# Performance work log

Measured on AMD Instinct MI355X. Metric: run time of the kernel, lower is better.

Reference implementation:

```python
import jax, jax.numpy as jnp
import numpy as np
import math

B, T, C = 2, 8192, 1024
H = 16
HD = C // H  # 64
WIN = 256    # local_window_size


def _rope_tables(T, hd):
    inv_freq = 1.0 / (10000.0 ** (np.arange(0, hd, 2, dtype=np.float32) / hd))
    t = np.arange(T, dtype=np.float32)
    freqs = np.outer(t, inv_freq)                      # [T, hd/2]
    emb = np.concatenate([freqs, freqs], axis=-1)      # [T, hd]
    return jnp.asarray(np.cos(emb))[None, None], jnp.asarray(np.sin(emb))[None, None]


def setup_inputs() -> dict:
    key = jax.random.key(0)
    ks = jax.random.split(key, 10)
    x = jax.random.normal(ks[0], (B, T, C), dtype=jnp.float32)
    # padding_mask: bool [B,T]; per the source, True positions end up masked out of attention
    padding_mask = jax.random.randint(ks[1], (B, T), 0, 2).astype(bool)
    cos, sin = _rope_tables(T, HD)                     # [1,1,T,HD]
    s = 1.0 / math.sqrt(C)
    Wq = jax.random.normal(ks[2], (C, C), dtype=jnp.float32) * s
    bq = jnp.zeros((C,), dtype=jnp.float32)
    Wk = jax.random.normal(ks[3], (C, C), dtype=jnp.float32) * s
    bk = jnp.zeros((C,), dtype=jnp.float32)
    Wv = jax.random.normal(ks[4], (C, C), dtype=jnp.float32) * s
    bv = jnp.zeros((C,), dtype=jnp.float32)
    Wo = jax.random.normal(ks[5], (C, C), dtype=jnp.float32) * s
    bo = jnp.zeros((C,), dtype=jnp.float32)
    return {"x": x, "padding_mask": padding_mask, "cos": cos, "sin": sin,
            "Wq": Wq, "bq": bq, "Wk": Wk, "bk": bk, "Wv": Wv, "bv": bv,
            "Wo": Wo, "bo": bo}


def _rotate_half(t):
    h = t.shape[-1] // 2
    return jnp.concatenate([-t[..., h:], t[..., :h]], axis=-1)


def reference(x, padding_mask, cos, sin, Wq, bq, Wk, bk, Wv, bv, Wo, bo):
    Bx, Tx, Cx = x.shape
    Wn = WIN
    pad_end = (Wn - Tx % Wn) % Wn            # static python int
    Tp = Tx + pad_end
    nW = Tp // Wn
    half = Wn // 2
    hd = cos.shape[-1]

    cos_t = jnp.broadcast_to(cos[0, 0][None], (Bx, Tx, hd))
    sin_t = jnp.broadcast_to(sin[0, 0][None], (Bx, Tx, hd))
    if pad_end > 0:
        x = jnp.pad(x, ((0, 0), (0, pad_end), (0, 0)))
        padding_mask = jnp.pad(padding_mask, ((0, 0), (0, pad_end)))
        cos_t = jnp.pad(cos_t, ((0, 0), (0, pad_end), (0, 0)))
        sin_t = jnp.pad(sin_t, ((0, 0), (0, pad_end), (0, 0)))

    # non-overlapping query windows: [B*nW, W, C]
    q_win = x.reshape(Bx * nW, Wn, Cx)
    cos_q = cos_t.reshape(Bx * nW, Wn, hd)[:, None]   # [Bw,1,W,hd]
    sin_q = sin_t.reshape(Bx * nW, Wn, hd)[:, None]

    # overlapping key/value windows of size 2W, stride W
    x_ctx = jnp.pad(x, ((0, 0), (half, half), (0, 0)))
    cos_ctx = jnp.pad(cos_t, ((0, 0), (half, half), (0, 0)))
    sin_ctx = jnp.pad(sin_t, ((0, 0), (half, half), (0, 0)))
    pk = jnp.pad(padding_mask, ((0, 0), (half, half)))  # pad value False
    idx = jnp.arange(nW)[:, None] * Wn + jnp.arange(2 * Wn)[None, :]  # [nW, 2W]
    k_win = x_ctx[:, idx].reshape(Bx * nW, 2 * Wn, Cx)
    cos_k = cos_ctx[:, idx].reshape(Bx * nW, 2 * Wn, hd)[:, None]
    sin_k = sin_ctx[:, idx].reshape(Bx * nW, 2 * Wn, hd)[:, None]
    pk = pk[:, idx].reshape(Bx * nW, 2 * Wn)

    # attn_mask: True = attend (SDPA bool-mask convention)
    attn_mask = ~pk
    all_attend = jnp.all(attn_mask, axis=-1)
    attn_mask = attn_mask.at[:, 0].set(jnp.where(all_attend, False, attn_mask[:, 0]))

    Bw = Bx * nW
    q = (q_win @ Wq.T + bq).reshape(Bw, Wn, H, HD).transpose(0, 2, 1, 3)        # [Bw,H,W,hd]
    k = (k_win @ Wk.T + bk).reshape(Bw, 2 * Wn, H, HD).transpose(0, 2, 1, 3)    # [Bw,H,2W,hd]
    v = (k_win @ Wv.T + bv).reshape(Bw, 2 * Wn, H, HD).transpose(0, 2, 1, 3)

    q = q * cos_q + _rotate_half(q) * sin_q
    k = k * cos_k + _rotate_half(k) * sin_k

    scale = 1.0 / math.sqrt(HD)
    scores = jnp.einsum('bhqd,bhkd->bhqk', q, k) * scale                        # [Bw,H,W,2W]
    scores = jnp.where(attn_mask[:, None, None, :], scores, jnp.finfo(scores.dtype).min)
    attn = jax.nn.softmax(scores, axis=-1)
    out = jnp.einsum('bhqk,bhkd->bhqd', attn, v)
    out = out.transpose(0, 2, 1, 3).reshape(Bw, Wn, Cx)
    out = out @ Wo.T + bo
    out = out.reshape(Bx, nW * Wn, Cx)[:, :Tx]
    return out
```

## Files before the change

### kernel.cpp

```cpp
#include <hip/hip_runtime.h>
#include <hip/hip_bf16.h>
#include <stdint.h>

#define T_SEQ 8192
#define B_SZ 2
#define CDIM 1024
#define NH 16
#define HDIM 64
#define NW 32

typedef unsigned short ushort_t;
typedef __attribute__((ext_vector_type(8))) short short8;
typedef __attribute__((ext_vector_type(8))) unsigned short us8;
typedef __attribute__((ext_vector_type(4))) unsigned short us4;
typedef __attribute__((ext_vector_type(4))) float f32x4;

__device__ __forceinline__ unsigned short f2bf(float f) {
  union { float f; unsigned int u; } c; c.f = f;
  return (unsigned short)((c.u + 0x7FFFu + ((c.u >> 16) & 1u)) >> 16);
}
__device__ __forceinline__ unsigned pk2(float a, float b) {
  unsigned r;
  asm("v_cvt_pk_bf16_f32 %0, %1, %2" : "=v"(r) : "v"(a), "v"(b));
  return r;
}
__device__ __forceinline__ void gld16(void* lds, const void* g) {
  __builtin_amdgcn_global_load_lds(
      (const __attribute__((address_space(1))) void*)g,
      (__attribute__((address_space(3))) void*)lds, 16, 0, 0);
}

__global__ __launch_bounds__(256) void cvt_all(const float* __restrict__ x,
                                               const float* __restrict__ w0,
                                               const float* __restrict__ w1,
                                               const float* __restrict__ w2,
                                               const float* __restrict__ w3,
                                               ushort_t* __restrict__ xbf,
                                               ushort_t* __restrict__ wbf,
                                               int nx4)
{
  int i = blockIdx.x * 256 + threadIdx.x;
  const float* src;
  ushort_t* dst;
  int idx;
  if (i < nx4) {
    src = x; dst = xbf; idx = i;
  } else {
    int j = i - nx4;
    int mat = j >> 18;
    idx = j & 262143;
    src = (mat == 0) ? w0 : (mat == 1) ? w1 : (mat == 2) ? w2 : w3;
    dst = wbf + (size_t)mat * CDIM * CDIM;
  }
  float4 v = ((const float4*)src)[idx];
  ushort4 o;
  o.x = f2bf(v.x); o.y = f2bf(v.y); o.z = f2bf(v.z); o.w = f2bf(v.w);
  ((ushort4*)dst)[idx] = o;
}

__device__ __forceinline__ void gemm256_core(const ushort_t* __restrict__ A,
                                             const ushort_t* __restrict__ W,
                                             ushort_t* SH,
                                             int m0, int n0, int t, f32x4 acc[8][4])
{
  const int lane = t & 63;
  const int wv = t >> 6;
  const int wr = wv >> 2;
  const int wc = wv & 3;
  const int fr = lane & 15;
  const int quad = lane >> 4;

  ushort_t* As = SH;
  ushort_t* Bs = SH + 32768;

  const int sr8 = lane >> 3;
  const int scb = ((lane & 7) ^ sr8) * 8;
  const int srowb = wv * 8 + sr8;
  const ushort_t* Ag = A + (size_t)(m0 + srowb) * CDIM + scb;
  const ushort_t* Wg = W + (size_t)(n0 + srowb) * CDIM + scb;
  ushort_t* lA = As + srowb * 64 + (lane & 7) * 8;
  ushort_t* lB = Bs + srowb * 64 + (lane & 7) * 8;

#pragma unroll
  for (int p = 0; p < 4; p++) {
    gld16(lA + p * 4096, Ag + (size_t)p * 64 * CDIM);
    gld16(lB + p * 4096, Wg + (size_t)p * 64 * CDIM);
  }
  __syncthreads();

  for (int kt = 0; kt < CDIM / 64; ++kt) {
    const int cur = kt & 1;
    if (kt + 1 < CDIM / 64) {
      const ushort_t* Agn = Ag + (kt + 1) * 64;
      const ushort_t* Wgn = Wg + (kt + 1) * 64;
      ushort_t* nA = lA + (cur ^ 1) * 16384;
      ushort_t* nB = lB + (cur ^ 1) * 16384;
#pragma unroll
      for (int p = 0; p < 4; p++) {
        gld16(nA + p * 4096, Agn + (size_t)p * 64 * CDIM);
        gld16(nB + p * 4096, Wgn + (size_t)p * 64 * CDIM);
      }
    }
    const ushort_t* Ac = As + cur * 16384;
    const ushort_t* Bc = Bs + cur * 16384;
    short8 b[4][2];
#pragma unroll
    for (int j = 0; j < 4; j++)
#pragma unroll
      for (int ks = 0; ks < 2; ks++)
        b[j][ks] = *(const short8*)&Bc[(wc * 64 + j * 16 + fr) * 64 +
                                       (((ks * 4 + quad) ^ (fr & 7)) * 8)];
    __builtin_amdgcn_s_setprio(1);
#pragma unroll
    for (int i = 0; i < 8; i++) {
      const int ra = (wr * 128 + i * 16 + fr) * 64;
      short8 a0 = *(const short8*)&Ac[ra + ((quad ^ (fr & 7)) * 8)];
      short8 a1 = *(const short8*)&Ac[ra + (((4 + quad) ^ (fr & 7)) * 8)];
#pragma unroll
      for (int j = 0; j < 4; j++)
        acc[i][j] = __builtin_amdgcn_mfma_f32_16x16x32_bf16(a0, b[j][0], acc[i][j], 0, 0, 0);
#pragma unroll
      for (int j = 0; j < 4; j++)
        acc[i][j] = __builtin_amdgcn_mfma_f32_16x16x32_bf16(a1, b[j][1], acc[i][j], 0, 0, 0);
    }
    __builtin_amdgcn_s_setprio(0);
    __syncthreads();
  }
}

__device__ __forceinline__ void xcd_swz(int& bx, int& by) {
  int gx = gridDim.x, nwg = gx * gridDim.y;
  int lid = bx + gx * by;
  int cpx = nwg >> 3;
  int swz = (lid & 7) * cpx + (lid >> 3);
  bx = swz % gx;
  by = swz / gx;
}

__global__ __launch_bounds__(512, 1) void gemm_qkv(const ushort_t* __restrict__ A,
                                                   const ushort_t* __restrict__ Wcat,
                                                   const float* __restrict__ bq,
                                                   const float* __restrict__ bk,
                                                   const float* __restrict__ bv,
                                                   ushort_t* __restrict__ Qb,
                                                   ushort_t* __restrict__ Kb,
                                                   ushort_t* __restrict__ Vtb,
                                                   const float* __restrict__ cosT,
                                                   const float* __restrict__ sinT)
{
  extern __shared__ ushort_t SH[];

  const int t = threadIdx.x;
  const int lane = t & 63;
  const int wv = t >> 6;
  const int wr = wv >> 2;
  const int wc = wv & 3;
  const int fr = lane & 15;
  const int quad = lane >> 4;
  int bx = blockIdx.x, by = blockIdx.y;
  xcd_swz(bx, by);
  const int m0 = by * 256;
  const int n0 = bx * 256;
  const int sec = bx >> 2;
  const int nsec0 = (bx & 3) * 256;
  const float* bias = (sec == 0) ? bq : (sec == 1) ? bk : bv;

  f32x4 acc[8][4];
#pragma unroll
  for (int i = 0; i < 8; i++)
#pragma unroll
    for (int j = 0; j < 4; j++) acc[i][j] = (f32x4){0.f, 0.f, 0.f, 0.f};

  gemm256_core(A, Wcat, SH, m0, n0, t, acc);

  if (sec < 2) {
    ushort_t* OutQK = sec ? Kb : Qb;
#pragma unroll
    for (int half = 0; half < 2; ++half) {
      if (wr == half) {
#pragma unroll
        for (int jp = 0; jp < 2; jp++) {
          int d = jp * 16 + fr;
          int cl = wc * 64 + jp * 16 + fr;
          float bl = bias[nsec0 + cl];
          float bh = bias[nsec0 + cl + 32];
#pragma unroll
          for (int i = 0; i < 8; i++) {
            int rloc = i * 16 + quad * 4;
#pragma unroll
            for (int r = 0; r < 4; r++) {
              int m = m0 + half * 128 + rloc + r;
              int tt = m & (T_SEQ - 1);
              float c = cosT[tt * HDIM + d];
              float sn = sinT[tt * HDIM + d];
              float lo = acc[i][jp][r] + bl;
              float hi = acc[i][jp + 2][r] + bh;
              SH[(rloc + r) * 264 + cl] = f2bf(lo * c - hi * sn);
              SH[(rloc + r) * 264 + cl + 32] = f2bf(hi * c + lo * sn);
            }
          }
        }
      }
      __syncthreads();
      const int rr0 = t >> 5;
      const int c8 = (t & 31) * 8;
      size_t gbase = (size_t)(m0 + half * 128) * CDIM + nsec0 + c8;
#pragma unroll
      for (int pp = 0; pp < 8; pp++) {
        int rr = pp * 16 + rr0;
        *(us8*)&OutQK[gbase + (size_t)rr * CDIM] = *(const us8*)&SH[rr * 264 + c8];
      }
      __syncthreads();
    }
  } else {
#pragma unroll
    for (int j = 0; j < 4; j++) {
      int ch = nsec0 + wc * 64 + j * 16 + fr;
      float bvv = bias[ch];
#pragma unroll
      for (int i = 0; i < 8; i++) {
        int m = m0 + wr * 128 + i * 16 + quad * 4;
        int bb = m >> 13;
        int tq = m & (T_SEQ - 1);
        us4 pk;
#pragma unroll
        for (int r = 0; r < 4; r++) pk[r] = f2bf(acc[i][j][r] + bvv);
        *(us4*)&Vtb[((size_t)bb * CDIM + ch) * T_SEQ + tq] = pk;
      }
    }
  }
}

__global__ __launch_bounds__(512, 1) void gemm_out(const ushort_t* __restrict__ A,
                                                   const ushort_t* __restrict__ W,
                                                   const float* __restrict__ bias,
                                                   float* __restrict__ Out)
{
  extern __shared__ ushort_t SH[];

  const int t = threadIdx.x;
  const int lane = t & 63;
  const int wv = t >> 6;
  const int wr = wv >> 2;
  const int wc = wv & 3;
  const int fr = lane & 15;
  const int quad = lane >> 4;
  int bx = blockIdx.x, by = blockIdx.y;
  xcd_swz(bx, by);
  const int m0 = by * 256;
  const int n0 = bx * 256;

  f32x4 acc[8][4];
#pragma unroll
  for (int i = 0; i < 8; i++)
#pragma unroll
    for (int j = 0; j < 4; j++) acc[i][j] = (f32x4){0.f, 0.f, 0.f, 0.f};

  gemm256_core(A, W, SH, m0, n0, t, acc);

#pragma unroll
  for (int j = 0; j < 4; j++) {
    int n = n0 + wc * 64 + j * 16 + fr;
    float bvv = bias[n];
#pragma unroll
    for (int i = 0; i < 8; i++) {
      int m = m0 + wr * 128 + i * 16 + quad * 4;
#pragma unroll
      for (int r = 0; r < 4; r++)
        Out[(size_t)(m + r) * CDIM + n] = acc[i][j][r] + bvv;
    }
  }
}

__global__ __launch_bounds__(256, 4) void attn_kernel(const ushort_t* __restrict__ Q,
                                                      const ushort_t* __restrict__ Kg,
                                                      const ushort_t* __restrict__ Vt,
                                                      const int* __restrict__ mask,
                                                      ushort_t* __restrict__ AO)
{
  __shared__ ushort_t Ks[64 * 72];
  __shared__ ushort_t Vts[64 * 72];
  __shared__ unsigned int PsW[4 * 32 * 32];
  __shared__ float attf[512];

  const int t = threadIdx.x;
  const int lane = t & 63;
  const int wv = t >> 6;
  const int h = blockIdx.x;
  const int w = blockIdx.y >> 1;
  const int qh = blockIdx.y & 1;
  const int b = blockIdx.z;
  const int fr = lane & 15;
  const int quad = lane >> 4;

  {
    int p0 = w * 256 + t - 128;
    bool a0 = (p0 < 0 || p0 >= T_SEQ) ? true : (mask[b * T_SEQ + p0] == 0);
    int p1 = p0 + 256;
    bool a1 = (p1 < 0 || p1 >= T_SEQ) ? true : (mask[b * T_SEQ + p1] == 0);
    int all1 = __syncthreads_and((int)(a0 && a1));
    attf[t] = a0 ? 0.f : -1.0e38f;
    attf[t + 256] = a1 ? 0.f : -1.0e38f;
    if (all1 && t == 0) attf[0] = -1.0e38f;
  }

  short8 qf[2][2];
  {
    const ushort_t* qp = Q + ((size_t)b * T_SEQ + w * 256 + qh * 128 + wv * 32 + fr) * CDIM
                           + h * HDIM + quad * 8;
#pragma unroll
    for (int mt = 0; mt < 2; mt++)
#pragma unroll
      for (int ks = 0; ks < 2; ks++)
        qf[mt][ks] = *(const short8*)&qp[(size_t)mt * 16 * CDIM + ks * 32];
  }

  const int srow = t >> 3;
  const int sc8 = (t & 7) * 8;
  const ushort_t* kgb = Kg + (size_t)b * T_SEQ * CDIM + h * HDIM + sc8;
  const ushort_t* vt_base = Vt + ((size_t)b * CDIM + h * HDIM) * T_SEQ;
  const float SCL = 0.18033688011112042f;

  unsigned int* pw = &PsW[wv * 1024];
  const int swz = (fr & 7) << 2;
  const int rbase = quad << 2;

  float m_run[2], l_run[2];
  f32x4 o[2][4];
#pragma unroll
  for (int mt = 0; mt < 2; mt++) { m_run[mt] = -3.0e38f; l_run[mt] = 0.f; }
#pragma unroll
  for (int mt = 0; mt < 2; mt++)
#pragma unroll
    for (int nt = 0; nt < 4; nt++) o[mt][nt] = (f32x4){0.f, 0.f, 0.f, 0.f};

  for (int kc = 0; kc < 8; kc++) {
    __syncthreads();
    {
#pragma unroll
      for (int p = 0; p < 2; p++) {
        int jj = p * 32 + srow;
        int pos = w * 256 + kc * 64 + jj - 128;
        us8 kval = (us8)(0);
        if (pos >= 0 && pos < T_SEQ) kval = *(const us8*)&kgb[(size_t)pos * CDIM];
        *(us8*)&Ks[jj * 72 + sc8] = kval;
      }
      int pos0 = w * 256 + kc * 64 - 128 + sc8;
      bool inr = (pos0 >= 0) && (pos0 < T_SEQ);
#pragma unroll
      for (int p = 0; p < 2; p++) {
        int d = p * 32 + srow;
        us8 vv = (us8)(0);
        if (inr) vv = *(const us8*)&vt_base[(size_t)d * T_SEQ + pos0];
        *(us8*)&Vts[d * 72 + sc8] = vv;
      }
    }
    __syncthreads();

    short8 kf[4][2];
#pragma unroll
    for (int nt = 0; nt < 4; nt++)
#pragma unroll
      for (int ks = 0; ks < 2; ks++)
        kf[nt][ks] = *(const short8*)&Ks[(nt * 16 + fr) * 72 + ks * 32 + quad * 8];

    f32x4 st[2][4];
    __builtin_amdgcn_s_setprio(1);
#pragma unroll
    for (int mt = 0; mt < 2; mt++)
#pragma unroll
      for (int nt = 0; nt < 4; nt++) {
        f32x4 a = (f32x4){0.f, 0.f, 0.f, 0.f};
        a = __builtin_amdgcn_mfma_f32_16x16x32_bf16(kf[nt][0], qf[mt][0], a, 0, 0, 0);
        a = __builtin_amdgcn_mfma_f32_16x16x32_bf16(kf[nt][1], qf[mt][1], a, 0, 0, 0);
        st[mt][nt] = a;
      }
    __builtin_amdgcn_s_setprio(0);

    f32x4 kb[4];
#pragma unroll
    for (int nt = 0; nt < 4; nt++)
      kb[nt] = *(const f32x4*)&attf[kc * 64 + nt * 16 + quad * 4];
#pragma unroll
    for (int mt = 0; mt < 2; mt++)
#pragma unroll
      for (int nt = 0; nt < 4; nt++)
#pragma unroll
        for (int r = 0; r < 4; r++)
          st[mt][nt][r] = __builtin_fmaf(st[mt][nt][r], SCL, kb[nt][r]);

#pragma unroll
    for (int mt = 0; mt < 2; mt++) {
      float t0 = fmaxf(fmaxf(st[mt][0][0], st[mt][0][1]), fmaxf(st[mt][0][2], st[mt][0][3]));
      float t1 = fmaxf(fmaxf(st[mt][1][0], st[mt][1][1]), fmaxf(st[mt][1][2], st[mt][1][3]));
      float t2 = fmaxf(fmaxf(st[mt][2][0], st[mt][2][1]), fmaxf(st[mt][2][2], st[mt][2][3]));
      float t3 = fmaxf(fmaxf(st[mt][3][0], st[mt][3][1]), fmaxf(st[mt][3][2], st[mt][3][3]));
      float mx = fmaxf(fmaxf(t0, t1), fmaxf(t2, t3));
      mx = fmaxf(mx, __shfl_xor(mx, 16, 64));
      mx = fmaxf(mx, __shfl_xor(mx, 32, 64));
      if (!__all(mx <= m_run[mt] + 8.f)) {
        float mnew = fmaxf(m_run[mt], mx);
        float alpha = __builtin_amdgcn_exp2f(m_run[mt] - mnew);
        m_run[mt] = mnew;
        l_run[mt] *= alpha;
        float af[4];
#pragma unroll
        for (int r = 0; r < 4; r++) af[r] = __shfl(alpha, rbase + r, 64);
#pragma unroll
        for (int nt = 0; nt < 4; nt++)
#pragma unroll
          for (int r = 0; r < 4; r++) o[mt][nt][r] *= af[r];
      }
      float rs = 0.f;
#pragma unroll
      for (int nt = 0; nt < 4; nt++)
#pragma unroll
        for (int r = 0; r < 4; r++) {
          float p = __builtin_amdgcn_exp2f(st[mt][nt][r] - m_run[mt]);
          st[mt][nt][r] = p;
          rs += p;
        }
      rs += __shfl_xor(rs, 16, 64);
      rs += __shfl_xor(rs, 32, 64);
      l_run[mt] += rs;

      unsigned int* pr = pw + ((mt * 16 + fr) << 5);
#pragma unroll
      for (int nt = 0; nt < 4; nt++)
#pragma unroll
        for (int hh = 0; hh < 2; hh++)
          pr[(((nt << 3) + (quad << 1) + hh)) ^ swz] =
              pk2(st[mt][nt][2 * hh], st[mt][nt][2 * hh + 1]);
    }

    short8 vf[4][2];
#pragma unroll
    for (int nt = 0; nt < 4; nt++)
#pragma unroll
      for (int ks = 0; ks < 2; ks++)
        vf[nt][ks] = *(const short8*)&Vts[(nt * 16 + fr) * 72 + ks * 32 + quad * 8];

    __builtin_amdgcn_s_setprio(1);
#pragma unroll
    for (int mt = 0; mt < 2; mt++) {
      const unsigned int* pr = pw + ((mt * 16 + fr) << 5);
      short8 pf[2];
#pragma unroll
      for (int ks = 0; ks < 2; ks++)
        pf[ks] = *(const short8*)&pr[((ks << 4) + (quad << 2)) ^ swz];
#pragma unroll
      for (int nt = 0; nt < 4; nt++) {
        o[mt][nt] = __builtin_amdgcn_mfma_f32_16x16x32_bf16(pf[0], vf[nt][0], o[mt][nt], 0, 0, 0);
        o[mt][nt] = __builtin_amdgcn_mfma_f32_16x16x32_bf16(pf[1], vf[nt][1], o[mt][nt], 0, 0, 0);
      }
    }
    __builtin_amdgcn_s_setprio(0);
  }

  size_t obase = ((size_t)b * T_SEQ + w * 256 + qh * 128 + wv * 32) * CDIM + h * HDIM;
#pragma unroll
  for (int mt = 0; mt < 2; mt++)
#pragma unroll
    for (int r = 0; r < 4; r++) {
      float lv = __shfl(l_run[mt], rbase + r, 64);
      float iv = 1.0f / fmaxf(lv, 1e-30f);
      int row = mt * 16 + quad * 4 + r;
#pragma unroll
      for (int nt = 0; nt < 4; nt++)
        AO[obase + (size_t)row * CDIM + nt * 16 + fr] = f2bf(o[mt][nt][r] * iv);
    }
}

extern "C" void kernel_launch(void* const* d_in, const int* in_sizes, int n_in,
                              void* d_out, int out_size, void* d_ws, size_t ws_size,
                              hipStream_t stream)
{
  const float* x    = (const float*)d_in[0];
  const int*   pm   = (const int*)d_in[1];
  const float* cosT = (const float*)d_in[2];
  const float* sinT = (const float*)d_in[3];
  const float* Wq   = (const float*)d_in[4];
  const float* bq   = (const float*)d_in[5];
  const float* Wk   = (const float*)d_in[6];
  const float* bk   = (const float*)d_in[7];
  const float* Wv   = (const float*)d_in[8];
  const float* bv   = (const float*)d_in[9];
  const float* Wo   = (const float*)d_in[10];
  const float* bo   = (const float*)d_in[11];
  float* out = (float*)d_out;

  static bool attr_done = false;
  if (!attr_done) {
    hipFuncSetAttribute(reinterpret_cast<const void*>(gemm_qkv),
                        hipFuncAttributeMaxDynamicSharedMemorySize, 131072);
    hipFuncSetAttribute(reinterpret_cast<const void*>(gemm_out),
                        hipFuncAttributeMaxDynamicSharedMemorySize, 131072);
    attr_done = true;
  }

  const size_t NTOK = (size_t)B_SZ * T_SEQ;
  const size_t NELT = NTOK * CDIM;
  ushort_t* Kb  = (ushort_t*)d_out;
  ushort_t* xbf = (ushort_t*)d_out + NELT;
  char* ws = (char*)d_ws;
  ushort_t* Wbf = (ushort_t*)ws;
  ushort_t* Qb  = (ushort_t*)(ws + 4 * (size_t)CDIM * CDIM * 2);
  ushort_t* Vtb = Qb + NELT;
  ushort_t* AO  = Qb;

  const int nx4 = (int)(NELT / 4);
  const int nblk = (nx4 + 4 * (CDIM * CDIM / 4)) / 256;
  cvt_all<<<nblk, 256, 0, stream>>>(x, Wq, Wk, Wv, Wo, xbf, Wbf, nx4);

  gemm_qkv<<<dim3(12, (int)(NTOK / 256)), 512, 131072, stream>>>(
      xbf, Wbf, bq, bk, bv, Qb, Kb, Vtb, cosT, sinT);

  attn_kernel<<<dim3(NH, NW * 2, B_SZ), 256, 0, stream>>>(Qb, Kb, Vtb, pm, AO);

  gemm_out<<<dim3(4, (int)(NTOK / 256)), 512, 131072, stream>>>(
      AO, Wbf + 3 * (size_t)CDIM * CDIM, bo, out);
}
```

Before: 404.7 us.

## Prefetch two K-tiles ahead in GEMM mainloop with explicit vmcnt waits

```diff
diff --git a/kernel.cpp b/kernel.cpp
--- a/kernel.cpp
+++ b/kernel.cpp
@@ -86,45 +86,59 @@
     gld16(lA + p * 4096, Ag + (size_t)p * 64 * CDIM);
     gld16(lB + p * 4096, Wg + (size_t)p * 64 * CDIM);
   }
-  __syncthreads();
+#pragma unroll
+  for (int p = 0; p < 4; p++) {
+    gld16(lA + 16384 + p * 4096, Ag + (size_t)p * 64 * CDIM + 64);
+    gld16(lB + 16384 + p * 4096, Wg + (size_t)p * 64 * CDIM + 64);
+  }
 
   for (int kt = 0; kt < CDIM / 64; ++kt) {
     const int cur = kt & 1;
-    if (kt + 1 < CDIM / 64) {
-      const ushort_t* Agn = Ag + (kt + 1) * 64;
-      const ushort_t* Wgn = Wg + (kt + 1) * 64;
-      ushort_t* nA = lA + (cur ^ 1) * 16384;
-      ushort_t* nB = lB + (cur ^ 1) * 16384;
-#pragma unroll
-      for (int p = 0; p < 4; p++) {
-        gld16(nA + p * 4096, Agn + (size_t)p * 64 * CDIM);
-        gld16(nB + p * 4096, Wgn + (size_t)p * 64 * CDIM);
-      }
-    }
+    if (kt < CDIM / 64 - 1) asm volatile("s_waitcnt vmcnt(8)" ::: "memory");
+    else                    asm volatile("s_waitcnt vmcnt(0)" ::: "memory");
+    __builtin_amdgcn_s_barrier();
+    asm volatile("" ::: "memory");
+
     const ushort_t* Ac = As + cur * 16384;
     const ushort_t* Bc = Bs + cur * 16384;
-    short8 b[4][2];
+    short8 b[4][2], a[8][2];
 #pragma unroll
     for (int j = 0; j < 4; j++)
 #pragma unroll
       for (int ks = 0; ks < 2; ks++)
         b[j][ks] = *(const short8*)&Bc[(wc * 64 + j * 16 + fr) * 64 +
                                        (((ks * 4 + quad) ^ (fr & 7)) * 8)];
-    __builtin_amdgcn_s_setprio(1);
 #pragma unroll
     for (int i = 0; i < 8; i++) {
       const int ra = (wr * 128 + i * 16 + fr) * 64;
-      short8 a0 = *(const short8*)&Ac[ra + ((quad ^ (fr & 7)) * 8)];
-      short8 a1 = *(const short8*)&Ac[ra + (((4 + quad) ^ (fr & 7)) * 8)];
+      a[i][0] = *(const short8*)&Ac[ra + ((quad ^ (fr & 7)) * 8)];
+      a[i][1] = *(const short8*)&Ac[ra + (((4 + quad) ^ (fr & 7)) * 8)];
+    }
+    asm volatile("s_waitcnt lgkmcnt(0)" ::: "memory");
+    __builtin_amdgcn_s_barrier();
+    asm volatile("" ::: "memory");
+
+    if (kt + 2 < CDIM / 64) {
+      const int kc = (kt + 2) * 64;
+      ushort_t* nA = lA + cur * 16384;
+      ushort_t* nB = lB + cur * 16384;
+#pragma unroll
+      for (int p = 0; p < 4; p++) {
+        gld16(nA + p * 4096, Ag + (size_t)p * 64 * CDIM + kc);
+        gld16(nB + p * 4096, Wg + (size_t)p * 64 * CDIM + kc);
+      }
+    }
+    __builtin_amdgcn_s_setprio(1);
+#pragma unroll
+    for (int i = 0; i < 8; i++) {
 #pragma unroll
       for (int j = 0; j < 4; j++)
-        acc[i][j] = __builtin_amdgcn_mfma_f32_16x16x32_bf16(a0, b[j][0], acc[i][j], 0, 0, 0);
+        acc[i][j] = __builtin_amdgcn_mfma_f32_16x16x32_bf16(a[i][0], b[j][0], acc[i][j], 0, 0, 0);
 #pragma unroll
       for (int j = 0; j < 4; j++)
-        acc[i][j] = __builtin_amdgcn_mfma_f32_16x16x32_bf16(a1, b[j][1], acc[i][j], 0, 0, 0);
+        acc[i][j] = __builtin_amdgcn_mfma_f32_16x16x32_bf16(a[i][1], b[j][1], acc[i][j], 0, 0, 0);
     }
     __builtin_amdgcn_s_setprio(0);
-    __syncthreads();
   }
 }
 
```

Measured after the change: 410.2 us. Within noise of the previous version (+1.4%).
